# Optimization experiments

Hardware: AMD Instinct MI355X
Metric: run time of the kernel (lower is better)

## Reference

```python
import jax, jax.numpy as jnp
import numpy as np

N = 100000   # nodes
E = 1600000  # edges (before self loops)
IN, HID, HEADS, OUT = 128, 32, 2, 32


def setup_inputs() -> dict:
    key = jax.random.key(0)
    ks = jax.random.split(key, 10)
    def glorot(k, shape, fan_in):
        return jax.random.normal(k, shape, dtype=jnp.float32) / np.sqrt(fan_in)
    return {
        "x": jax.random.normal(ks[0], (N, IN), dtype=jnp.float32),
        "edge_index": jax.random.randint(ks[1], (2, E), 0, N, dtype=jnp.int32),
        "W1": glorot(ks[2], (IN, HEADS * HID), IN),
        "a_src1": glorot(ks[3], (HEADS, HID), HID),
        "a_dst1": glorot(ks[4], (HEADS, HID), HID),
        "b1": jnp.zeros((HEADS * HID,), dtype=jnp.float32),
        "W2": glorot(ks[5], (HEADS * HID, OUT), HEADS * HID),
        "a_src2": glorot(ks[6], (1, OUT), OUT),
        "a_dst2": glorot(ks[7], (1, OUT), OUT),
        "b2": jnp.zeros((OUT,), dtype=jnp.float32),
    }


def gat_conv(x, W, a_src, a_dst, b, src, dst, n):
    """PyG-style GATConv: shared linear, edge softmax over incoming edges, sum aggregate."""
    H, C = a_src.shape
    xl = (x @ W).reshape(n, H, C)                       # [N, H, C]
    asn = jnp.einsum('nhc,hc->nh', xl, a_src)            # per-node source score
    adn = jnp.einsum('nhc,hc->nh', xl, a_dst)            # per-node dest score
    e = jax.nn.leaky_relu(asn[src] + adn[dst], 0.2)      # [E', H]
    m = jax.ops.segment_max(e, dst, num_segments=n)      # stable softmax per dest
    m = jnp.where(jnp.isfinite(m), m, 0.0)
    ex = jnp.exp(e - m[dst])
    denom = jax.ops.segment_sum(ex, dst, num_segments=n)
    alpha = ex / (denom[dst] + 1e-16)                    # [E', H]
    out = jax.ops.segment_sum(xl[src] * alpha[:, :, None], dst, num_segments=n)
    return out.reshape(n, H * C) + b


def reference(x, edge_index, W1, a_src1, a_dst1, b1, W2, a_src2, a_dst2, b2):
    n = x.shape[0]
    loop = jnp.arange(n, dtype=edge_index.dtype)         # add self loops (PyG default)
    src = jnp.concatenate([edge_index[0], loop])
    dst = jnp.concatenate([edge_index[1], loop])
    h = jax.nn.relu(gat_conv(x, W1, a_src1, a_dst1, b1, src, dst, n))
    # F.dropout(p=0.5) is identity in eval mode
    return gat_conv(h, W2, a_src2, a_dst2, b2, src, dst, n)
```

## Files before the change

kernel.cpp:

```cpp
#include <hip/hip_runtime.h>
#include <hip/hip_fp16.h>


#define BS 256
#define PCHUNK 8192
#define CAPB 5632
#define GPAD 16

typedef _Float16 half8 __attribute__((ext_vector_type(8)));
typedef float f32x4 __attribute__((ext_vector_type(4)));

__global__ __launch_bounds__(BS) void k_init(int* __restrict__ gcursor, int nbuk) {
    for (int i = threadIdx.x; i < nbuk; i += BS) gcursor[i * GPAD] = i * CAPB;
}

__global__ __launch_bounds__(BS) void k_pg1(const int* __restrict__ ei, int E, int n,
                                            int* __restrict__ gcursor, int* __restrict__ ppair,
                                            const float* __restrict__ x, const float* __restrict__ W,
                                            const float* __restrict__ asrc, const float* __restrict__ adst,
                                            __half* __restrict__ xl, float* __restrict__ sc, int gC) {
    __shared__ _Float16 smem[8192];
    int tid = threadIdx.x;
    if ((int)blockIdx.x < gC) {
        int* cnt  = (int*)smem;
        int* gpos = cnt + 512;
        int* lcur = cnt + 1024;
        cnt[tid] = 0; cnt[tid + 256] = 0;
        lcur[tid] = 0; lcur[tid + 256] = 0;
        __syncthreads();
        const int* dstp = ei + E;
        int base = blockIdx.x * PCHUNK;
        bool full = (base + PCHUNK <= E);
        if (full) {
            const int4* dv = (const int4*)(dstp + base) + tid * 8;
#pragma unroll
            for (int k = 0; k < 8; k++) {
                int4 d4 = dv[k];
                atomicAdd(&cnt[d4.x >> 8], 1);
                atomicAdd(&cnt[d4.y >> 8], 1);
                atomicAdd(&cnt[d4.z >> 8], 1);
                atomicAdd(&cnt[d4.w >> 8], 1);
            }
        } else {
            for (int i = tid; base + i < E; i += BS)
                atomicAdd(&cnt[dstp[base + i] >> 8], 1);
        }
        __syncthreads();
        for (int b = tid; b < 512; b += BS) {
            int c = cnt[b];
            if (c > 0) gpos[b] = atomicAdd(&gcursor[b * GPAD], c);
        }
        __syncthreads();
        if (full) {
            const int4* sv = (const int4*)(ei + base) + tid * 8;
            const int4* dv = (const int4*)(dstp + base) + tid * 8;
#pragma unroll 2
            for (int k = 0; k < 8; k++) {
                int4 s4 = sv[k];
                int4 d4 = dv[k];
                int d, s, b, r;
                d = d4.x; s = s4.x; b = d >> 8; r = atomicAdd(&lcur[b], 1);
                ppair[gpos[b] + r] = ((d & 255) << 17) | s;
                d = d4.y; s = s4.y; b = d >> 8; r = atomicAdd(&lcur[b], 1);
                ppair[gpos[b] + r] = ((d & 255) << 17) | s;
                d = d4.z; s = s4.z; b = d >> 8; r = atomicAdd(&lcur[b], 1);
                ppair[gpos[b] + r] = ((d & 255) << 17) | s;
                d = d4.w; s = s4.w; b = d >> 8; r = atomicAdd(&lcur[b], 1);
                ppair[gpos[b] + r] = ((d & 255) << 17) | s;
            }
        } else {
            for (int i = tid; base + i < E; i += BS) {
                int s = ei[base + i], d = dstp[base + i];
                int b = d >> 8;
                int r = atomicAdd(&lcur[b], 1);
                ppair[gpos[b] + r] = ((d & 255) << 17) | s;
            }
        }
        return;
    }
    _Float16* wf = smem;
    for (int i = tid; i < 8192; i += BS) {
        int j = i & 7, ln = (i >> 3) & 63, f = i >> 9;
        int kt = f >> 2, nt = f & 3;
        int k = kt * 32 + (ln >> 4) * 8 + j;
        wf[i] = (_Float16)W[k * 64 + nt * 16 + (ln & 15)];
    }
    __syncthreads();
    int wave = tid >> 6, lane = tid & 63;
    int nb = ((blockIdx.x - gC) * 4 + wave) * 16;
    int m = lane & 15, q = lane >> 4;
    int node_m = nb + m; if (node_m >= n) node_m = n - 1;
    half8 bf[4][4];
#pragma unroll
    for (int f = 0; f < 16; f++)
        bf[f >> 2][f & 3] = *(half8*)&wf[(f * 64 + lane) * 8];
    f32x4 acc[4] = {f32x4{0,0,0,0}, f32x4{0,0,0,0}, f32x4{0,0,0,0}, f32x4{0,0,0,0}};
#pragma unroll
    for (int kt = 0; kt < 4; kt++) {
        const float* xp = x + (size_t)node_m * 128 + kt * 32 + q * 8;
        float4 xa = *(const float4*)xp;
        float4 xb = *(const float4*)(xp + 4);
        half8 a;
        a[0] = (_Float16)xa.x; a[1] = (_Float16)xa.y; a[2] = (_Float16)xa.z; a[3] = (_Float16)xa.w;
        a[4] = (_Float16)xb.x; a[5] = (_Float16)xb.y; a[6] = (_Float16)xb.z; a[7] = (_Float16)xb.w;
#pragma unroll
        for (int nt = 0; nt < 4; nt++)
            acc[nt] = __builtin_amdgcn_mfma_f32_16x16x32_f16(a, bf[kt][nt], acc[nt], 0, 0, 0);
    }
    int c = lane & 15;
    float a_s[4], a_d[4];
#pragma unroll
    for (int nt = 0; nt < 4; nt++) { a_s[nt] = asrc[nt * 16 + c]; a_d[nt] = adst[nt * 16 + c]; }
#pragma unroll
    for (int r = 0; r < 4; r++) {
        int node = nb + q * 4 + r;
        bool ok = node < n;
        float v0 = acc[0][r], v1 = acc[1][r], v2 = acc[2][r], v3 = acc[3][r];
        float as0 = v0 * a_s[0] + v1 * a_s[1];
        float as1 = v2 * a_s[2] + v3 * a_s[3];
        float ad0 = v0 * a_d[0] + v1 * a_d[1];
        float ad1 = v2 * a_d[2] + v3 * a_d[3];
#pragma unroll
        for (int off = 1; off < 16; off <<= 1) {
            as0 += __shfl_xor(as0, off); as1 += __shfl_xor(as1, off);
            ad0 += __shfl_xor(ad0, off); ad1 += __shfl_xor(ad1, off);
        }
        if (ok) {
            __half* row = xl + (size_t)node * 64;
            row[c]      = __float2half(v0);
            row[16 + c] = __float2half(v1);
            row[32 + c] = __float2half(v2);
            row[48 + c] = __float2half(v3);
            if (c == 0) ((float4*)sc)[node] = make_float4(as0, as1, ad0, ad1);
        }
    }
}

__global__ __launch_bounds__(BS) void k_bucket(const int* __restrict__ ppair,
                                               const int* __restrict__ gcursor, int n,
                                               int* __restrict__ col,
                                               int* __restrict__ row_ptr, int* __restrict__ row_end) {
    __shared__ int ldeg[256];
    __shared__ int lscan[256];
    __shared__ int lcur[256];
    __shared__ int lcol[CAPB];
    int b = blockIdx.x;
    int t = threadIdx.x;
    int lo = b << 8;
    int hi = lo + 256; if (hi > n) hi = n;
    int W = hi - lo;
    int base = b * CAPB;
    int cnt = gcursor[b * GPAD] - base;
    if (cnt > CAPB) cnt = CAPB;
    ldeg[t] = 0;
    __syncthreads();
    for (int i = t; i < cnt; i += BS)
        atomicAdd(&ldeg[ppair[base + i] >> 17], 1);
    __syncthreads();
    lscan[t] = ldeg[t];
    __syncthreads();
    for (int off = 1; off < 256; off <<= 1) {
        int a = (t >= off) ? lscan[t - off] : 0;
        __syncthreads();
        lscan[t] += a;
        __syncthreads();
    }
    {
        int e0 = lscan[t] - ldeg[t];
        lcur[t] = e0;
        if (t < W) { row_ptr[lo + t] = base + e0; row_end[lo + t] = base + e0 + ldeg[t]; }
    }
    __syncthreads();
    for (int i = t; i < cnt; i += BS) {
        int p = ppair[base + i];
        int r = atomicAdd(&lcur[p >> 17], 1);
        if (r < CAPB) lcol[r] = p & 131071;
    }
    __syncthreads();
    for (int i = t; i < cnt; i += BS) col[base + i] = lcol[i];
}

__global__ __launch_bounds__(BS) void k_ag1g2(const int* __restrict__ row_ptr, const int* __restrict__ row_end,
                                              const int* __restrict__ col, const __half* __restrict__ xl,
                                              const float* __restrict__ sc, const float* __restrict__ asrc,
                                              const float* __restrict__ b1,
                                              const float* __restrict__ W2,
                                              const float* __restrict__ as2, const float* __restrict__ ad2,
                                              __half* __restrict__ xl2, float* __restrict__ sc2, int n) {
    __shared__ _Float16 hsh[32 * 72];
    __shared__ _Float16 wf2[2048];
    int tid = threadIdx.x;
    for (int i = tid; i < 2048; i += BS) {
        int j = i & 7, ln = (i >> 3) & 63, f = i >> 9;
        int kt = f >> 1, nt = f & 1;
        int k = kt * 32 + (ln >> 4) * 8 + j;
        wf2[i] = (_Float16)W2[k * 32 + nt * 16 + (ln & 15)];
    }
    int node_local = tid >> 3;
    int node = blockIdx.x * 32 + node_local;
    int tc = tid & 7;
    int lane = tid & 63;
    int tb = lane & 56;
    bool alive = node < n;
    int nodeC = alive ? node : n - 1;
    float4 acA = ((const float4*)asrc)[tc * 2];
    float4 acB = ((const float4*)asrc)[tc * 2 + 1];
    int s0 = row_ptr[nodeC], e1 = row_end[nodeC];
    float4 sn = ((const float4*)sc)[nodeC];
    bool hh0 = tc < 4;
    float adn = hh0 ? sn.z : sn.w;
    float es0 = sn.x + sn.z; es0 = fmaxf(es0, 0.2f * es0);
    float es1 = sn.y + sn.w; es1 = fmaxf(es1, 0.2f * es1);
    float xs = __expf(hh0 ? es0 : es1);
    uint4 rawS = *(const uint4*)(xl + (size_t)nodeC * 64 + tc * 8);
    __half2 sh0 = *(__half2*)&rawS.x, sh1 = *(__half2*)&rawS.y;
    __half2 sh2 = *(__half2*)&rawS.z, sh3 = *(__half2*)&rawS.w;
    float acc0 = xs * __low2float(sh0), acc1 = xs * __high2float(sh0);
    float acc2 = xs * __low2float(sh1), acc3 = xs * __high2float(sh1);
    float acc4 = xs * __low2float(sh2), acc5 = xs * __high2float(sh2);
    float acc6 = xs * __low2float(sh3), acc7 = xs * __high2float(sh3);
    float den = xs;
    int deg = e1 - s0;
    int mx = deg;
    mx = max(mx, __shfl_xor(mx, 8));
    mx = max(mx, __shfl_xor(mx, 16));
    mx = max(mx, __shfl_xor(mx, 32));
    int nch = (mx + 7) >> 3;
    for (int ci = 0; ci < nch; ci++) {
        int pos = s0 + ci * 8;
        int m = e1 - pos; m = m < 0 ? 0 : (m > 8 ? 8 : m);
        int srcv = (tc < m) ? col[pos + tc] : 0;
#pragma unroll
        for (int k = 0; k < 8; k++) {
            if (k < m) {
                int sE = __shfl(srcv, tb + k);
                uint4 r = *(const uint4*)(xl + (size_t)sE * 64 + tc * 8);
                __half2 q0 = *(__half2*)&r.x, q1 = *(__half2*)&r.y;
                __half2 q2 = *(__half2*)&r.z, q3 = *(__half2*)&r.w;
                float f0 = __low2float(q0), f1 = __high2float(q0);
                float f2 = __low2float(q1), f3 = __high2float(q1);
                float f4 = __low2float(q2), f5 = __high2float(q2);
                float f6 = __low2float(q3), f7 = __high2float(q3);
                float dot = f0 * acA.x + f1 * acA.y + f2 * acA.z + f3 * acA.w
                          + f4 * acB.x + f5 * acB.y + f6 * acB.z + f7 * acB.w;
                dot += __shfl_xor(dot, 1);
                dot += __shfl_xor(dot, 2);
                float e = dot + adn; e = fmaxf(e, 0.2f * e);
                float w = __expf(e);
                acc0 = fmaf(w, f0, acc0); acc1 = fmaf(w, f1, acc1);
                acc2 = fmaf(w, f2, acc2); acc3 = fmaf(w, f3, acc3);
                acc4 = fmaf(w, f4, acc4); acc5 = fmaf(w, f5, acc5);
                acc6 = fmaf(w, f6, acc6); acc7 = fmaf(w, f7, acc7);
                den += w;
            }
        }
    }
    float dinv = 1.f / (den + 1e-16f);
    {
        float4 bvA = ((const float4*)b1)[tc * 2];
        float4 bvB = ((const float4*)b1)[tc * 2 + 1];
        __half2 p0 = __floats2half2_rn(fmaxf(fmaf(acc0, dinv, bvA.x), 0.f),
                                       fmaxf(fmaf(acc1, dinv, bvA.y), 0.f));
        __half2 p1 = __floats2half2_rn(fmaxf(fmaf(acc2, dinv, bvA.z), 0.f),
                                       fmaxf(fmaf(acc3, dinv, bvA.w), 0.f));
        __half2 p2 = __floats2half2_rn(fmaxf(fmaf(acc4, dinv, bvB.x), 0.f),
                                       fmaxf(fmaf(acc5, dinv, bvB.y), 0.f));
        __half2 p3 = __floats2half2_rn(fmaxf(fmaf(acc6, dinv, bvB.z), 0.f),
                                       fmaxf(fmaf(acc7, dinv, bvB.w), 0.f));
        uint4 o;
        o.x = *(unsigned int*)&p0; o.y = *(unsigned int*)&p1;
        o.z = *(unsigned int*)&p2; o.w = *(unsigned int*)&p3;
        *(uint4*)&hsh[node_local * 72 + tc * 8] = o;
    }
    __syncthreads();
    int wave = tid >> 6;
    if (wave < 2) {
        int m2 = lane & 15, q2 = lane >> 4;
        int nl = wave * 16 + m2;
        half8 bf[2][2];
#pragma unroll
        for (int f = 0; f < 4; f++)
            bf[f >> 1][f & 1] = *(half8*)&wf2[(f * 64 + lane) * 8];
        f32x4 acc2g[2] = {f32x4{0,0,0,0}, f32x4{0,0,0,0}};
#pragma unroll
        for (int kt = 0; kt < 2; kt++) {
            half8 a = *(half8*)&hsh[nl * 72 + kt * 32 + q2 * 8];
#pragma unroll
            for (int nt = 0; nt < 2; nt++)
                acc2g[nt] = __builtin_amdgcn_mfma_f32_16x16x32_f16(a, bf[kt][nt], acc2g[nt], 0, 0, 0);
        }
        int c = lane & 15;
        float a_s[2], a_d[2];
#pragma unroll
        for (int nt = 0; nt < 2; nt++) { a_s[nt] = as2[nt * 16 + c]; a_d[nt] = ad2[nt * 16 + c]; }
#pragma unroll
        for (int r = 0; r < 4; r++) {
            int nl_r = wave * 16 + q2 * 4 + r;
            int node_r = blockIdx.x * 32 + nl_r;
            bool ok = node_r < n;
            float v0 = acc2g[0][r], v1 = acc2g[1][r];
            float as = v0 * a_s[0] + v1 * a_s[1];
            float ad = v0 * a_d[0] + v1 * a_d[1];
#pragma unroll
            for (int off = 1; off < 16; off <<= 1) {
                as += __shfl_xor(as, off); ad += __shfl_xor(ad, off);
            }
            if (ok) {
                __half* row = xl2 + (size_t)node_r * 32;
                row[c]      = __float2half(v0);
                row[16 + c] = __float2half(v1);
                if (c == 0) ((float2*)sc2)[node_r] = make_float2(as, ad);
            }
        }
    }
}

__global__ __launch_bounds__(BS) void k_agg2(const int* __restrict__ row_ptr, const int* __restrict__ row_end,
                                             const int* __restrict__ col, const __half* __restrict__ xl,
                                             const float* __restrict__ sc, const float* __restrict__ asrc,
                                             const float* __restrict__ b2,
                                             float* __restrict__ out, int n) {
    int tid = blockIdx.x * BS + threadIdx.x;
    int node = tid >> 2;
    int tc = threadIdx.x & 3;
    int lane = threadIdx.x & 63;
    int tb = lane & 60;
    bool alive = node < n;
    if (!alive) node = n - 1;
    float4 acA = ((const float4*)asrc)[tc * 2];
    float4 acB = ((const float4*)asrc)[tc * 2 + 1];
    int s0 = row_ptr[node], e1 = row_end[node];
    float2 sn = ((const float2*)sc)[node];
    float adn = sn.y;
    float es = sn.x + adn; es = fmaxf(es, 0.2f * es);
    float xs = __expf(es);
    uint4 rawS = *(const uint4*)(xl + (size_t)node * 32 + tc * 8);
    __half2 sh0 = *(__half2*)&rawS.x, sh1 = *(__half2*)&rawS.y;
    __half2 sh2 = *(__half2*)&rawS.z, sh3 = *(__half2*)&rawS.w;
    float acc0 = xs * __low2float(sh0), acc1 = xs * __high2float(sh0);
    float acc2 = xs * __low2float(sh1), acc3 = xs * __high2float(sh1);
    float acc4 = xs * __low2float(sh2), acc5 = xs * __high2float(sh2);
    float acc6 = xs * __low2float(sh3), acc7 = xs * __high2float(sh3);
    float den = xs;
    int deg = e1 - s0;
    int mx = deg;
    mx = max(mx, __shfl_xor(mx, 4));
    mx = max(mx, __shfl_xor(mx, 8));
    mx = max(mx, __shfl_xor(mx, 16));
    mx = max(mx, __shfl_xor(mx, 32));
    int nch = (mx + 3) >> 2;
    for (int ci = 0; ci < nch; ci++) {
        int pos = s0 + ci * 4;
        int m = e1 - pos; m = m < 0 ? 0 : (m > 4 ? 4 : m);
        int srcv = (tc < m) ? col[pos + tc] : 0;
#pragma unroll
        for (int k = 0; k < 4; k++) {
            if (k < m) {
                int sE = __shfl(srcv, tb + k);
                uint4 r = *(const uint4*)(xl + (size_t)sE * 32 + tc * 8);
                __half2 q0 = *(__half2*)&r.x, q1 = *(__half2*)&r.y;
                __half2 q2 = *(__half2*)&r.z, q3 = *(__half2*)&r.w;
                float f0 = __low2float(q0), f1 = __high2float(q0);
                float f2 = __low2float(q1), f3 = __high2float(q1);
                float f4 = __low2float(q2), f5 = __high2float(q2);
                float f6 = __low2float(q3), f7 = __high2float(q3);
                float dot = f0 * acA.x + f1 * acA.y + f2 * acA.z + f3 * acA.w
                          + f4 * acB.x + f5 * acB.y + f6 * acB.z + f7 * acB.w;
                dot += __shfl_xor(dot, 1);
                dot += __shfl_xor(dot, 2);
                float e = dot + adn; e = fmaxf(e, 0.2f * e);
                float w = __expf(e);
                acc0 = fmaf(w, f0, acc0); acc1 = fmaf(w, f1, acc1);
                acc2 = fmaf(w, f2, acc2); acc3 = fmaf(w, f3, acc3);
                acc4 = fmaf(w, f4, acc4); acc5 = fmaf(w, f5, acc5);
                acc6 = fmaf(w, f6, acc6); acc7 = fmaf(w, f7, acc7);
                den += w;
            }
        }
    }
    float dinv = 1.f / (den + 1e-16f);
    if (alive) {
        float4 bvA = ((const float4*)b2)[tc * 2];
        float4 bvB = ((const float4*)b2)[tc * 2 + 1];
        float4 oA, oB;
        oA.x = fmaf(acc0, dinv, bvA.x);
        oA.y = fmaf(acc1, dinv, bvA.y);
        oA.z = fmaf(acc2, dinv, bvA.z);
        oA.w = fmaf(acc3, dinv, bvA.w);
        oB.x = fmaf(acc4, dinv, bvB.x);
        oB.y = fmaf(acc5, dinv, bvB.y);
        oB.z = fmaf(acc6, dinv, bvB.z);
        oB.w = fmaf(acc7, dinv, bvB.w);
        float4* orow = (float4*)(out + (size_t)node * 32);
        orow[tc * 2]     = oA;
        orow[tc * 2 + 1] = oB;
    }
}

extern "C" void kernel_launch(void* const* d_in, const int* in_sizes, int n_in,
                              void* d_out, int out_size, void* d_ws, size_t ws_size,
                              hipStream_t stream) {
    const float* x    = (const float*)d_in[0];
    const int*   ei   = (const int*)d_in[1];
    const float* W1   = (const float*)d_in[2];
    const float* as1  = (const float*)d_in[3];
    const float* ad1  = (const float*)d_in[4];
    const float* b1   = (const float*)d_in[5];
    const float* W2   = (const float*)d_in[6];
    const float* as2  = (const float*)d_in[7];
    const float* ad2  = (const float*)d_in[8];
    const float* b2   = (const float*)d_in[9];
    int n = in_sizes[0] / 128;
    int E = in_sizes[1] / 2;
    int NBUK = (n + 255) >> 8;

    char* w = (char*)d_ws;
    auto alloc = [&](size_t bytes) -> char* {
        char* p = w; w += (bytes + 255) / 256 * 256; return p;
    };
    int*    gcursor = (int*)alloc((size_t)NBUK * GPAD * 4);
    int*    ppair   = (int*)alloc((size_t)NBUK * CAPB * 4);
    int*    col     = (int*)alloc((size_t)NBUK * CAPB * 4);
    int*    row_ptr = (int*)alloc((size_t)n * 4);
    int*    row_end = (int*)alloc((size_t)n * 4);
    __half* xl1     = (__half*)alloc((size_t)n * 64 * 2);
    float*  sc1     = (float*)alloc((size_t)n * 4 * 4);
    __half* xl2     = (__half*)alloc((size_t)n * 32 * 2);
    float*  sc2     = (float*)alloc((size_t)n * 2 * 4);

    int gC  = (E + PCHUNK - 1) / PCHUNK;
    int gG  = (n + 63) / 64;
    int gA1 = (n * 8 + BS - 1) / BS;
    int gA2 = (n * 4 + BS - 1) / BS;

    k_init   <<<1, BS, 0, stream>>>(gcursor, NBUK);
    k_pg1    <<<gC + gG, BS, 0, stream>>>(ei, E, n, gcursor, ppair,
                                          x, W1, as1, ad1, xl1, sc1, gC);
    k_bucket <<<NBUK, BS, 0, stream>>>(ppair, gcursor, n, col, row_ptr, row_end);
    k_ag1g2  <<<gA1, BS, 0, stream>>>(row_ptr, row_end, col, xl1, sc1, as1, b1,
                                      W2, as2, ad2, xl2, sc2, n);
    k_agg2   <<<gA2, BS, 0, stream>>>(row_ptr, row_end, col, xl2, sc2, as2, b2,
                                      (float*)d_out, n);
}
```

Before: 220.6 us.

## Software-pipeline neighbor gathers with triple-buffered register prefetch in both GAT aggregations

The edge aggregation loops in both layers now issue gathers for the next two 4-edge groups into register buffers before consuming the current group. This hides gather latency by keeping more loads in flight per thread. In exchange it uses more VGPRs (three sets of four uint4 buffers), which may lower occupancy, and it reads col past the current group but within clamped bounds. Layer 1 also moves from 8-edge to 4-edge chunks.

```diff
diff --git a/kernel.cpp b/kernel.cpp
--- a/kernel.cpp
+++ b/kernel.cpp
@@ -225,36 +225,61 @@
     mx = max(mx, __shfl_xor(mx, 8));
     mx = max(mx, __shfl_xor(mx, 16));
     mx = max(mx, __shfl_xor(mx, 32));
-    int nch = (mx + 7) >> 3;
-    for (int ci = 0; ci < nch; ci++) {
-        int pos = s0 + ci * 8;
-        int m = e1 - pos; m = m < 0 ? 0 : (m > 8 ? 8 : m);
-        int srcv = (tc < m) ? col[pos + tc] : 0;
-#pragma unroll
-        for (int k = 0; k < 8; k++) {
-            if (k < m) {
-                int sE = __shfl(srcv, tb + k);
-                uint4 r = *(const uint4*)(xl + (size_t)sE * 64 + tc * 8);
-                __half2 q0 = *(__half2*)&r.x, q1 = *(__half2*)&r.y;
-                __half2 q2 = *(__half2*)&r.z, q3 = *(__half2*)&r.w;
-                float f0 = __low2float(q0), f1 = __high2float(q0);
-                float f2 = __low2float(q1), f3 = __high2float(q1);
-                float f4 = __low2float(q2), f5 = __high2float(q2);
-                float f6 = __low2float(q3), f7 = __high2float(q3);
-                float dot = f0 * acA.x + f1 * acA.y + f2 * acA.z + f3 * acA.w
-                          + f4 * acB.x + f5 * acB.y + f6 * acB.z + f7 * acB.w;
-                dot += __shfl_xor(dot, 1);
-                dot += __shfl_xor(dot, 2);
-                float e = dot + adn; e = fmaxf(e, 0.2f * e);
-                float w = __expf(e);
-                acc0 = fmaf(w, f0, acc0); acc1 = fmaf(w, f1, acc1);
-                acc2 = fmaf(w, f2, acc2); acc3 = fmaf(w, f3, acc3);
-                acc4 = fmaf(w, f4, acc4); acc5 = fmaf(w, f5, acc5);
-                acc6 = fmaf(w, f6, acc6); acc7 = fmaf(w, f7, acc7);
-                den += w;
-            }
-        }
-    }
+    int nq = (mx + 3) >> 2;
+
+    uint4 rrA[4], rrB[4], rrC[4];
+    int mA, mB, mC, svA, svB, svC;
+
+#define CLAMP4(Q) ({ int _m = deg - (Q) * 4; _m = _m < 0 ? 0 : (_m > 4 ? 4 : _m); _m; })
+#define LOADCOL(Q, M) ((tc < (M)) ? col[s0 + (Q) * 4 + tc] : 0)
+#define ISSUE1(RR, SV, M)                                               \
+    _Pragma("unroll")                                                   \
+    for (int k = 0; k < 4; k++) {                                       \
+        if (k < (M)) {                                                  \
+            int sE = __shfl((SV), tb + k);                              \
+            RR[k] = *(const uint4*)(xl + (size_t)sE * 64 + tc * 8);     \
+        }                                                               \
+    }
+#define CONSUME1(RR, M)                                                 \
+    _Pragma("unroll")                                                   \
+    for (int k = 0; k < 4; k++) {                                       \
+        if (k < (M)) {                                                  \
+            __half2 q0 = *(__half2*)&RR[k].x, q1 = *(__half2*)&RR[k].y; \
+            __half2 q2 = *(__half2*)&RR[k].z, q3 = *(__half2*)&RR[k].w; \
+            float f0 = __low2float(q0), f1 = __high2float(q0);          \
+            float f2 = __low2float(q1), f3 = __high2float(q1);          \
+            float f4 = __low2float(q2), f5 = __high2float(q2);          \
+            float f6 = __low2float(q3), f7 = __high2float(q3);          \
+            float dA = f0 * acA.x + f1 * acA.y + f2 * acA.z + f3 * acA.w; \
+            float dB = f4 * acB.x + f5 * acB.y + f6 * acB.z + f7 * acB.w; \
+            float dot = dA + dB;                                        \
+            dot += __shfl_xor(dot, 1);                                  \
+            dot += __shfl_xor(dot, 2);                                  \
+            float e = dot + adn; e = fmaxf(e, 0.2f * e);                \
+            float w = __expf(e);                                        \
+            acc0 = fmaf(w, f0, acc0); acc1 = fmaf(w, f1, acc1);         \
+            acc2 = fmaf(w, f2, acc2); acc3 = fmaf(w, f3, acc3);         \
+            acc4 = fmaf(w, f4, acc4); acc5 = fmaf(w, f5, acc5);         \
+            acc6 = fmaf(w, f6, acc6); acc7 = fmaf(w, f7, acc7);         \
+            den += w;                                                   \
+        }                                                               \
+    }
+
+    mA = CLAMP4(0); svA = LOADCOL(0, mA); ISSUE1(rrA, svA, mA);
+    mB = CLAMP4(1); svB = LOADCOL(1, mB); ISSUE1(rrB, svB, mB);
+    for (int q = 0; q < nq; q += 3) {
+        mC = CLAMP4(q + 2); svC = LOADCOL(q + 2, mC); ISSUE1(rrC, svC, mC);
+        CONSUME1(rrA, mA);
+        mA = CLAMP4(q + 3); svA = LOADCOL(q + 3, mA); ISSUE1(rrA, svA, mA);
+        CONSUME1(rrB, mB);
+        mB = CLAMP4(q + 4); svB = LOADCOL(q + 4, mB); ISSUE1(rrB, svB, mB);
+        CONSUME1(rrC, mC);
+    }
+#undef CLAMP4
+#undef LOADCOL
+#undef ISSUE1
+#undef CONSUME1
+
     float dinv = 1.f / (den + 1e-16f);
     {
         float4 bvA = ((const float4*)b1)[tc * 2];
@@ -348,36 +373,61 @@
     mx = max(mx, __shfl_xor(mx, 8));
     mx = max(mx, __shfl_xor(mx, 16));
     mx = max(mx, __shfl_xor(mx, 32));
-    int nch = (mx + 3) >> 2;
-    for (int ci = 0; ci < nch; ci++) {
-        int pos = s0 + ci * 4;
-        int m = e1 - pos; m = m < 0 ? 0 : (m > 4 ? 4 : m);
-        int srcv = (tc < m) ? col[pos + tc] : 0;
-#pragma unroll
-        for (int k = 0; k < 4; k++) {
-            if (k < m) {
-                int sE = __shfl(srcv, tb + k);
-                uint4 r = *(const uint4*)(xl + (size_t)sE * 32 + tc * 8);
-                __half2 q0 = *(__half2*)&r.x, q1 = *(__half2*)&r.y;
-                __half2 q2 = *(__half2*)&r.z, q3 = *(__half2*)&r.w;
-                float f0 = __low2float(q0), f1 = __high2float(q0);
-                float f2 = __low2float(q1), f3 = __high2float(q1);
-                float f4 = __low2float(q2), f5 = __high2float(q2);
-                float f6 = __low2float(q3), f7 = __high2float(q3);
-                float dot = f0 * acA.x + f1 * acA.y + f2 * acA.z + f3 * acA.w
-                          + f4 * acB.x + f5 * acB.y + f6 * acB.z + f7 * acB.w;
-                dot += __shfl_xor(dot, 1);
-                dot += __shfl_xor(dot, 2);
-                float e = dot + adn; e = fmaxf(e, 0.2f * e);
-                float w = __expf(e);
-                acc0 = fmaf(w, f0, acc0); acc1 = fmaf(w, f1, acc1);
-                acc2 = fmaf(w, f2, acc2); acc3 = fmaf(w, f3, acc3);
-                acc4 = fmaf(w, f4, acc4); acc5 = fmaf(w, f5, acc5);
-                acc6 = fmaf(w, f6, acc6); acc7 = fmaf(w, f7, acc7);
-                den += w;
-            }
-        }
-    }
+    int nq = (mx + 3) >> 2;
+
+    uint4 rrA[4], rrB[4], rrC[4];
+    int mA, mB, mC, svA, svB, svC;
+
+#define CLAMP4(Q) ({ int _m = deg - (Q) * 4; _m = _m < 0 ? 0 : (_m > 4 ? 4 : _m); _m; })
+#define LOADCOL(Q, M) ((tc < (M)) ? col[s0 + (Q) * 4 + tc] : 0)
+#define ISSUE2(RR, SV, M)                                               \
+    _Pragma("unroll")                                                   \
+    for (int k = 0; k < 4; k++) {                                       \
+        if (k < (M)) {                                                  \
+            int sE = __shfl((SV), tb + k);                              \
+            RR[k] = *(const uint4*)(xl + (size_t)sE * 32 + tc * 8);     \
+        }                                                               \
+    }
+#define CONSUME2(RR, M)                                                 \
+    _Pragma("unroll")                                                   \
+    for (int k = 0; k < 4; k++) {                                       \
+        if (k < (M)) {                                                  \
+            __half2 q0 = *(__half2*)&RR[k].x, q1 = *(__half2*)&RR[k].y; \
+            __half2 q2 = *(__half2*)&RR[k].z, q3 = *(__half2*)&RR[k].w; \
+            float f0 = __low2float(q0), f1 = __high2float(q0);          \
+            float f2 = __low2float(q1), f3 = __high2float(q1);          \
+            float f4 = __low2float(q2), f5 = __high2float(q2);          \
+            float f6 = __low2float(q3), f7 = __high2float(q3);          \
+            float dA = f0 * acA.x + f1 * acA.y + f2 * acA.z + f3 * acA.w; \
+            float dB = f4 * acB.x + f5 * acB.y + f6 * acB.z + f7 * acB.w; \
+            float dot = dA + dB;                                        \
+            dot += __shfl_xor(dot, 1);                                  \
+            dot += __shfl_xor(dot, 2);                                  \
+            float e = dot + adn; e = fmaxf(e, 0.2f * e);                \
+            float w = __expf(e);                                        \
+            acc0 = fmaf(w, f0, acc0); acc1 = fmaf(w, f1, acc1);         \
+            acc2 = fmaf(w, f2, acc2); acc3 = fmaf(w, f3, acc3);         \
+            acc4 = fmaf(w, f4, acc4); acc5 = fmaf(w, f5, acc5);         \
+            acc6 = fmaf(w, f6, acc6); acc7 = fmaf(w, f7, acc7);         \
+            den += w;                                                   \
+        }                                                               \
+    }
+
+    mA = CLAMP4(0); svA = LOADCOL(0, mA); ISSUE2(rrA, svA, mA);
+    mB = CLAMP4(1); svB = LOADCOL(1, mB); ISSUE2(rrB, svB, mB);
+    for (int q = 0; q < nq; q += 3) {
+        mC = CLAMP4(q + 2); svC = LOADCOL(q + 2, mC); ISSUE2(rrC, svC, mC);
+        CONSUME2(rrA, mA);
+        mA = CLAMP4(q + 3); svA = LOADCOL(q + 3, mA); ISSUE2(rrA, svA, mA);
+        CONSUME2(rrB, mB);
+        mB = CLAMP4(q + 4); svB = LOADCOL(q + 4, mB); ISSUE2(rrB, svB, mB);
+        CONSUME2(rrC, mC);
+    }
+#undef CLAMP4
+#undef LOADCOL
+#undef ISSUE2
+#undef CONSUME2
+
     float dinv = 1.f / (den + 1e-16f);
     if (alive) {
         float4 bvA = ((const float4*)b2)[tc * 2];
```

Result: slower. 254.7 us (+15.4%).
